# Performance work log

Hardware: AMD Instinct MI355X
Metric: run time of the kernel (lower is better)

Reference implementation:

```python
import jax, jax.numpy as jnp
import numpy as np
import math

DIM, HEAD_DIM = 1024, 64
N_HEADS = DIM // HEAD_DIM
B, S = 8, 1025
EPS = 1e-5


def _make_theta():
    # freqs: geometric between pi and 10*pi
    log_min, log_max = math.log(math.pi), math.log(10 * math.pi)
    n = N_HEADS * HEAD_DIM // 4
    freqs = np.exp(np.linspace(log_min, log_max, n + 1, dtype=np.float64)[:-1]).astype(np.float32)
    freqs = freqs.reshape(HEAD_DIM // 4, N_HEADS).T  # (H, D/4)
    # axial positions on a 32x32 grid, with one zero row prepended -> 1025 rows
    h_pos = np.linspace(-1, 1, 33, dtype=np.float32)
    h_pos = (h_pos[:-1] + h_pos[1:]) / 2
    hh, ww = np.meshgrid(h_pos, h_pos, indexing='ij')
    pos = np.stack([hh, ww], axis=-1).reshape(32 * 32, 2)
    pos = np.concatenate([np.zeros((1, 2), np.float32), pos], axis=0)  # (1025, 2)
    theta_h = pos[:, None, 0:1] * freqs  # (1025, H, D/4)
    theta_w = pos[:, None, 1:2] * freqs
    return jnp.asarray(np.concatenate([theta_h, theta_w], axis=-1))  # (1025, H, D/2)


def _rope(x, theta):
    # x: (B,H,S,D); theta: (B,H,S,d) with d = D//2
    d = theta.shape[-1]
    x1, x2, rest = x[..., :d], x[..., d:2 * d], x[..., 2 * d:]
    cos, sin = jnp.cos(theta), jnp.sin(theta)
    y1 = x1 * cos - x2 * sin
    y2 = x2 * cos + x1 * sin
    return jnp.concatenate([y1, y2, rest], axis=-1)


def setup_inputs() -> dict:
    key = jax.random.key(0)
    ks = jax.random.split(key, 8)
    x = jax.random.normal(ks[0], (B, S, DIM), jnp.float32)
    pos = jax.random.randint(ks[1], (B, S), 0, 1025)
    s = 1.0 / math.sqrt(DIM)
    return {
        'x': x,
        'pos': pos,
        'theta': _make_theta(),
        'ln_w': jnp.ones((DIM,), jnp.float32),
        'ln_b': jnp.zeros((DIM,), jnp.float32),
        'qkv_w': jax.random.normal(ks[2], (3 * DIM, DIM), jnp.float32) * s,
        'qkv_b': jnp.zeros((3 * DIM,), jnp.float32),
        'out_w': jax.random.normal(ks[3], (DIM, DIM), jnp.float32) * (s * 0.02),
        'out_b': jnp.zeros((DIM,), jnp.float32),
    }


def reference(x, pos, theta, ln_w, ln_b, qkv_w, qkv_b, out_w, out_b):
    b, s, dim = x.shape
    # LayerNorm
    mu = jnp.mean(x, axis=-1, keepdims=True)
    var = jnp.mean(jnp.square(x - mu), axis=-1, keepdims=True)
    h = (x - mu) * jax.lax.rsqrt(var + EPS) * ln_w + ln_b
    # QKV projection -> (B, S, 3, H, D)
    qkv = (h @ qkv_w.T + qkv_b).reshape(b, s, 3, N_HEADS, HEAD_DIM)
    q = qkv[:, :, 0].transpose(0, 2, 1, 3)  # (B,H,S,D)
    k = qkv[:, :, 1].transpose(0, 2, 1, 3)
    v = qkv[:, :, 2].transpose(0, 2, 1, 3)
    # Rotary: theta[pos] -> (B,S,H,d) -> (B,H,S,d)
    th = theta[pos].transpose(0, 2, 1, 3)
    q = _rope(q, th)
    k = _rope(k, th)
    # causal SDPA
    scale = 1.0 / math.sqrt(HEAD_DIM)
    scores = jnp.einsum('bhqd,bhkd->bhqk', q, k) * scale
    causal = jnp.tril(jnp.ones((s, s), bool))
    scores = jnp.where(causal, scores, jnp.finfo(scores.dtype).min)
    attn = jax.nn.softmax(scores, axis=-1)
    o = jnp.einsum('bhqk,bhkd->bhqd', attn, v)
    o = o.transpose(0, 2, 1, 3).reshape(b, s, dim)
    return o @ out_w.T + out_b
```

## Files before the change

### kernel.cpp

```cpp
#include <hip/hip_runtime.h>
#include <math.h>

#define B_SZ 8
#define S_LEN 1025
#define DIM 1024
#define NH 16
#define HD 64
#define QKV_DIM 3072
#define M_ROWS (B_SZ * S_LEN)

typedef __attribute__((ext_vector_type(8))) short bf16x8;
typedef __attribute__((ext_vector_type(4))) float f32x4;

__device__ __forceinline__ unsigned short f2bf(float x) {
  unsigned u = __float_as_uint(x);
  unsigned r = u + 0x7FFFu + ((u >> 16) & 1u);
  return (unsigned short)(r >> 16);
}
__device__ __forceinline__ float bf2f(unsigned short h) {
  return __uint_as_float(((unsigned)h) << 16);
}

__device__ __forceinline__ int lds_addr(int row, int byte_in_row) {
  return row * 128 + (byte_in_row & 15) + ((((byte_in_row >> 4) ^ row) & 7) << 4);
}

__device__ __forceinline__ void cvt_write8(char* hi, char* lo, const float* f) {
  union { unsigned short us[8]; uint4 q; } H, L;
  #pragma unroll
  for (int i = 0; i < 8; ++i) {
    unsigned short h = f2bf(f[i]);
    H.us[i] = h;
    L.us[i] = f2bf(f[i] - bf2f(h));
  }
  *(uint4*)hi = H.q;
  *(uint4*)lo = L.q;
}

__global__ __launch_bounds__(256) void ln_kernel(const float* __restrict__ x,
                                                 const float* __restrict__ w,
                                                 const float* __restrict__ b,
                                                 float* __restrict__ h) {
  const int row = blockIdx.x;
  const int t = threadIdx.x;
  const float* xr = x + (size_t)row * DIM;
  float4 v = *(const float4*)(xr + t * 4);
  float s  = v.x + v.y + v.z + v.w;
  float s2 = v.x * v.x + v.y * v.y + v.z * v.z + v.w * v.w;
  #pragma unroll
  for (int off = 32; off > 0; off >>= 1) {
    s  += __shfl_down(s, off);
    s2 += __shfl_down(s2, off);
  }
  __shared__ float red[10];
  const int wid = t >> 6;
  if ((t & 63) == 0) { red[wid] = s; red[4 + wid] = s2; }
  __syncthreads();
  if (t == 0) {
    float ts = 0.f, ts2 = 0.f;
    #pragma unroll
    for (int i = 0; i < 4; ++i) { ts += red[i]; ts2 += red[4 + i]; }
    float mu  = ts * (1.0f / DIM);
    float var = ts2 * (1.0f / DIM) - mu * mu;
    red[8] = mu;
    red[9] = rsqrtf(var + 1e-5f);
  }
  __syncthreads();
  const float mu = red[8], rs = red[9];
  float4 wv = *(const float4*)(w + t * 4);
  float4 bv = *(const float4*)(b + t * 4);
  float4 o;
  o.x = (v.x - mu) * rs * wv.x + bv.x;
  o.y = (v.y - mu) * rs * wv.y + bv.y;
  o.z = (v.z - mu) * rs * wv.z + bv.z;
  o.w = (v.w - mu) * rs * wv.w + bv.w;
  *(float4*)(h + (size_t)row * DIM + t * 4) = o;
}

__global__ __launch_bounds__(256) void gemm_bf16x3(const float* __restrict__ A,
                                                   const float* __restrict__ B,
                                                   const float* __restrict__ bias,
                                                   float* __restrict__ C,
                                                   int M, int N, int K) {
  __shared__ char lds[65536];
  char* Ahi = lds;
  char* Alo = lds + 16384;
  char* Bhi = lds + 32768;
  char* Blo = lds + 49152;

  const int t = threadIdx.x;
  const int l = t & 63;
  const int wid = t >> 6;
  const int wrow = (wid & 1) * 64;
  const int wcol = (wid >> 1) * 64;
  const int m0 = blockIdx.x * 128;
  const int n0 = blockIdx.y * 128;

  const f32x4 zero = {0.f, 0.f, 0.f, 0.f};
  f32x4 acc[4][4];
  #pragma unroll
  for (int i = 0; i < 4; ++i)
    #pragma unroll
    for (int j = 0; j < 4; ++j) acc[i][j] = zero;

  const int kc = (t & 7) * 8;
  const int lrow = (l & 15);
  const int lch = (l >> 4);

  for (int k0 = 0; k0 < K; k0 += 64) {
    __syncthreads();
    float va[4][8], vb[4][8];
    #pragma unroll
    for (int p = 0; p < 4; ++p) {
      const int row = p * 32 + (t >> 3);
      const int m = m0 + row;
      if (m < M) {
        const float* pa = A + (size_t)m * K + k0 + kc;
        *(float4*)&va[p][0] = *(const float4*)pa;
        *(float4*)&va[p][4] = *(const float4*)(pa + 4);
      } else {
        #pragma unroll
        for (int i = 0; i < 8; ++i) va[p][i] = 0.f;
      }
      const float* pb = B + (size_t)(n0 + row) * K + k0 + kc;
      *(float4*)&vb[p][0] = *(const float4*)pb;
      *(float4*)&vb[p][4] = *(const float4*)(pb + 4);
    }
    #pragma unroll
    for (int p = 0; p < 4; ++p) {
      const int row = p * 32 + (t >> 3);
      const int a = lds_addr(row, kc * 2);
      cvt_write8(Ahi + a, Alo + a, va[p]);
      cvt_write8(Bhi + a, Blo + a, vb[p]);
    }
    __syncthreads();
    #pragma unroll
    for (int ks = 0; ks < 2; ++ks) {
      const int bycol = ks * 64 + lch * 16;
      bf16x8 ah[4], al[4], bh[4], bl[4];
      #pragma unroll
      for (int rt = 0; rt < 4; ++rt) {
        const int ar = lds_addr(wrow + rt * 16 + lrow, bycol);
        ah[rt] = *(const bf16x8*)(Ahi + ar);
        al[rt] = *(const bf16x8*)(Alo + ar);
        const int br = lds_addr(wcol + rt * 16 + lrow, bycol);
        bh[rt] = *(const bf16x8*)(Bhi + br);
        bl[rt] = *(const bf16x8*)(Blo + br);
      }
      #pragma unroll
      for (int rt = 0; rt < 4; ++rt)
        #pragma unroll
        for (int ct = 0; ct < 4; ++ct) {
          acc[rt][ct] = __builtin_amdgcn_mfma_f32_16x16x32_bf16(ah[rt], bh[ct], acc[rt][ct], 0, 0, 0);
          acc[rt][ct] = __builtin_amdgcn_mfma_f32_16x16x32_bf16(ah[rt], bl[ct], acc[rt][ct], 0, 0, 0);
          acc[rt][ct] = __builtin_amdgcn_mfma_f32_16x16x32_bf16(al[rt], bh[ct], acc[rt][ct], 0, 0, 0);
        }
    }
  }

  #pragma unroll
  for (int rt = 0; rt < 4; ++rt)
    #pragma unroll
    for (int ct = 0; ct < 4; ++ct) {
      const int n = n0 + wcol + ct * 16 + lrow;
      const float bv = bias[n];
      #pragma unroll
      for (int j = 0; j < 4; ++j) {
        const int m = m0 + wrow + rt * 16 + lch * 4 + j;
        if (m < M) C[(size_t)m * N + n] = acc[rt][ct][j] + bv;
      }
    }
}

__global__ __launch_bounds__(256) void rope_kernel(float* __restrict__ qkv,
                                                   const int* __restrict__ pos,
                                                   const float* __restrict__ theta) {
  const int id = blockIdx.x * 256 + threadIdx.x;
  if (id >= B_SZ * S_LEN * NH * 32) return;
  const int d  = id & 31;
  const int hh = (id >> 5) & 15;
  const int bs = id >> 9;
  const int p = pos[bs];
  const float th = theta[((size_t)p * NH + hh) * 32 + d];
  float sn, c;
  sincosf(th, &sn, &c);
  const size_t base = (size_t)bs * QKV_DIM + hh * HD + d;
  #pragma unroll
  for (int tt = 0; tt < 2; ++tt) {
    const size_t i1 = base + tt * DIM;
    float x1 = qkv[i1];
    float x2 = qkv[i1 + 32];
    qkv[i1]      = x1 * c - x2 * sn;
    qkv[i1 + 32] = x2 * c + x1 * sn;
  }
}

__global__ __launch_bounds__(256) void attn_mfma(const float* __restrict__ qkv,
                                                 float* __restrict__ o_out) {
  const int qt = blockIdx.x;
  const int hh = blockIdx.y;
  const int b  = blockIdx.z;
  const int t  = threadIdx.x;
  const int l  = t & 63;
  const int w  = t >> 6;
  const int q0 = qt * 64;
  const int lrow = l & 15;
  const int lch  = l >> 4;

  __shared__ char lds[49152];
  char* Khi  = lds;
  char* Klo  = lds + 8192;
  char* Vthi = lds + 16384;
  char* Vtlo = lds + 24576;
  char* Phi  = lds + 32768;
  char* Plo  = lds + 40960;

  const size_t bs_base = (size_t)b * S_LEN * QKV_DIM;

  bf16x8 qh[2], ql[2];
  {
    const int qrow = q0 + w * 16 + lrow;
    #pragma unroll
    for (int ks = 0; ks < 2; ++ks) {
      float f[8];
      if (qrow < S_LEN) {
        const float* p = qkv + bs_base + (size_t)qrow * QKV_DIM + hh * HD + ks * 32 + lch * 8;
        *(float4*)&f[0] = *(const float4*)p;
        *(float4*)&f[4] = *(const float4*)(p + 4);
      } else {
        #pragma unroll
        for (int i = 0; i < 8; ++i) f[i] = 0.f;
      }
      union { unsigned short us[8]; bf16x8 v; } H, L;
      #pragma unroll
      for (int i = 0; i < 8; ++i) {
        const float x = f[i] * 0.125f;
        unsigned short hi = f2bf(x);
        H.us[i] = hi;
        L.us[i] = f2bf(x - bf2f(hi));
      }
      qh[ks] = H.v;
      ql[ks] = L.v;
    }
  }

  const f32x4 zero = {0.f, 0.f, 0.f, 0.f};
  f32x4 acc[4];
  float m[4], lsum[4];
  #pragma unroll
  for (int ct = 0; ct < 4; ++ct) acc[ct] = zero;
  #pragma unroll
  for (int j = 0; j < 4; ++j) { m[j] = -1e30f; lsum[j] = 0.f; }

  const int kt_max = (q0 + 63 < S_LEN ? q0 + 63 : S_LEN - 1) >> 6;
  const int sr = t >> 2;
  const int sg = t & 3;

  for (int kt = 0; kt <= kt_max; ++kt) {
    const int k0 = kt * 64;
    __syncthreads();
    {
      float kf[16], vf[16];
      const int s = k0 + sr;
      if (s < S_LEN) {
        const float* base = qkv + bs_base + (size_t)s * QKV_DIM + hh * HD + sg * 16;
        #pragma unroll
        for (int q = 0; q < 4; ++q) {
          *(float4*)&kf[q * 4] = *(const float4*)(base + DIM + q * 4);
          *(float4*)&vf[q * 4] = *(const float4*)(base + 2 * DIM + q * 4);
        }
      } else {
        #pragma unroll
        for (int i = 0; i < 16; ++i) { kf[i] = 0.f; vf[i] = 0.f; }
      }
      const int a0 = lds_addr(sr, sg * 32);
      const int a1 = lds_addr(sr, sg * 32 + 16);
      cvt_write8(Khi + a0, Klo + a0, kf);
      cvt_write8(Khi + a1, Klo + a1, kf + 8);
      #pragma unroll
      for (int i = 0; i < 16; ++i) {
        const int ad = lds_addr(sg * 16 + i, sr * 2);
        unsigned short hi = f2bf(vf[i]);
        *(unsigned short*)(Vthi + ad) = hi;
        *(unsigned short*)(Vtlo + ad) = f2bf(vf[i] - bf2f(hi));
      }
    }
    __syncthreads();

    f32x4 sc[4];
    #pragma unroll
    for (int ct = 0; ct < 4; ++ct) {
      f32x4 s = zero;
      #pragma unroll
      for (int ks = 0; ks < 2; ++ks) {
        const int off = lds_addr(ct * 16 + lrow, ks * 64 + lch * 16);
        bf16x8 kh = *(const bf16x8*)(Khi + off);
        bf16x8 kl = *(const bf16x8*)(Klo + off);
        s = __builtin_amdgcn_mfma_f32_16x16x32_bf16(qh[ks], kh, s, 0, 0, 0);
        s = __builtin_amdgcn_mfma_f32_16x16x32_bf16(qh[ks], kl, s, 0, 0, 0);
        s = __builtin_amdgcn_mfma_f32_16x16x32_bf16(ql[ks], kh, s, 0, 0, 0);
      }
      sc[ct] = s;
    }

    #pragma unroll
    for (int ct = 0; ct < 4; ++ct) {
      const int kj = k0 + lrow + ct * 16;
      #pragma unroll
      for (int j = 0; j < 4; ++j) {
        const int qi = q0 + w * 16 + lch * 4 + j;
        if (kj > qi) sc[ct][j] = -1e30f;
      }
    }

    float tmax[4];
    #pragma unroll
    for (int j = 0; j < 4; ++j)
      tmax[j] = fmaxf(fmaxf(sc[0][j], sc[1][j]), fmaxf(sc[2][j], sc[3][j]));
    #pragma unroll
    for (int off = 1; off < 16; off <<= 1)
      #pragma unroll
      for (int j = 0; j < 4; ++j)
        tmax[j] = fmaxf(tmax[j], __shfl_xor(tmax[j], off, 16));

    float mnew[4], tsum[4];
    #pragma unroll
    for (int j = 0; j < 4; ++j) {
      mnew[j] = fmaxf(m[j], tmax[j]);
      float su = 0.f;
      #pragma unroll
      for (int ct = 0; ct < 4; ++ct) {
        sc[ct][j] = __expf(sc[ct][j] - mnew[j]);
        su += sc[ct][j];
      }
      tsum[j] = su;
    }
    #pragma unroll
    for (int off = 1; off < 16; off <<= 1)
      #pragma unroll
      for (int j = 0; j < 4; ++j) tsum[j] += __shfl_xor(tsum[j], off, 16);
    #pragma unroll
    for (int j = 0; j < 4; ++j) {
      const float co = __expf(m[j] - mnew[j]);
      lsum[j] = lsum[j] * co + tsum[j];
      #pragma unroll
      for (int ct = 0; ct < 4; ++ct) acc[ct][j] *= co;
      m[j] = mnew[j];
    }

    #pragma unroll
    for (int ct = 0; ct < 4; ++ct)
      #pragma unroll
      for (int j = 0; j < 4; ++j) {
        const float pv = sc[ct][j];
        const int ad = lds_addr(w * 16 + lch * 4 + j, (lrow + ct * 16) * 2);
        unsigned short hi = f2bf(pv);
        *(unsigned short*)(Phi + ad) = hi;
        *(unsigned short*)(Plo + ad) = f2bf(pv - bf2f(hi));
      }
    __syncthreads();

    #pragma unroll
    for (int ks = 0; ks < 2; ++ks) {
      const int poff = lds_addr(w * 16 + lrow, ks * 64 + lch * 16);
      bf16x8 ph = *(const bf16x8*)(Phi + poff);
      bf16x8 pl = *(const bf16x8*)(Plo + poff);
      #pragma unroll
      for (int ct = 0; ct < 4; ++ct) {
        const int voff = lds_addr(ct * 16 + lrow, ks * 64 + lch * 16);
        bf16x8 vh = *(const bf16x8*)(Vthi + voff);
        bf16x8 vl = *(const bf16x8*)(Vtlo + voff);
        acc[ct] = __builtin_amdgcn_mfma_f32_16x16x32_bf16(ph, vh, acc[ct], 0, 0, 0);
        acc[ct] = __builtin_amdgcn_mfma_f32_16x16x32_bf16(ph, vl, acc[ct], 0, 0, 0);
        acc[ct] = __builtin_amdgcn_mfma_f32_16x16x32_bf16(pl, vh, acc[ct], 0, 0, 0);
      }
    }
  }

  #pragma unroll
  for (int j = 0; j < 4; ++j) {
    const int s = q0 + w * 16 + lch * 4 + j;
    if (s >= S_LEN) continue;
    const float inv = 1.f / lsum[j];
    #pragma unroll
    for (int ct = 0; ct < 4; ++ct)
      o_out[((size_t)b * S_LEN + s) * DIM + hh * HD + lrow + ct * 16] = acc[ct][j] * inv;
  }
}

extern "C" void kernel_launch(void* const* d_in, const int* in_sizes, int n_in,
                              void* d_out, int out_size, void* d_ws, size_t ws_size,
                              hipStream_t stream) {
  const float* x     = (const float*)d_in[0];
  const int*   pos   = (const int*)d_in[1];
  const float* theta = (const float*)d_in[2];
  const float* ln_w  = (const float*)d_in[3];
  const float* ln_b  = (const float*)d_in[4];
  const float* qkv_w = (const float*)d_in[5];
  const float* qkv_b = (const float*)d_in[6];
  const float* out_w = (const float*)d_in[7];
  const float* out_b = (const float*)d_in[8];
  float* out = (float*)d_out;

  float* h   = (float*)d_ws;
  float* qkv = h + (size_t)M_ROWS * DIM;
  float* o   = h;

  ln_kernel<<<M_ROWS, 256, 0, stream>>>(x, ln_w, ln_b, h);
  gemm_bf16x3<<<dim3(65, 24), 256, 0, stream>>>(h, qkv_w, qkv_b, qkv,
                                                M_ROWS, QKV_DIM, DIM);
  rope_kernel<<<(B_SZ * S_LEN * NH * 32 + 255) / 256, 256, 0, stream>>>(qkv, pos, theta);
  attn_mfma<<<dim3(17, NH, B_SZ), 256, 0, stream>>>(qkv, o);
  gemm_bf16x3<<<dim3(65, 8), 256, 0, stream>>>(o, out_w, out_b, out,
                                               M_ROWS, DIM, DIM);
}
```

Baseline: 632.2 us.

## Store intermediates as pre-split bf16 hi/lo planes across all kernels

LayerNorm, the QKV GEMM epilogue, rope and attention output now write activations as separate bf16 hi and lo planes, not fp32. Consumers load these planes straight into LDS and skip the per-tile fp32-to-bf16x2 split, which cuts conversion ALU work in the GEMM and attention K/V loading loops. The Q scale moves from the Q load to the scores. Total bytes per element stay the same, but the QKV epilogue does uncoalesced 2-byte stores and rope does extra split work.

```diff
diff --git a/kernel.cpp b/kernel.cpp
--- a/kernel.cpp
+++ b/kernel.cpp
@@ -1,4 +1,5 @@
 #include <hip/hip_runtime.h>
+#include <hip/hip_bf16.h>
 #include <math.h>
 
 #define B_SZ 8
@@ -11,13 +12,15 @@
 
 typedef __attribute__((ext_vector_type(8))) short bf16x8;
 typedef __attribute__((ext_vector_type(4))) float f32x4;
-
-__device__ __forceinline__ unsigned short f2bf(float x) {
-  unsigned u = __float_as_uint(x);
-  unsigned r = u + 0x7FFFu + ((u >> 16) & 1u);
-  return (unsigned short)(r >> 16);
-}
-__device__ __forceinline__ float bf2f(unsigned short h) {
+typedef unsigned short u16;
+
+__device__ __forceinline__ void bsplit(float x, u16& hi, u16& lo) {
+  __hip_bfloat16 bh = __float2bfloat16(x);
+  __builtin_memcpy(&hi, &bh, 2);
+  __hip_bfloat16 bl = __float2bfloat16(x - __bfloat162float(bh));
+  __builtin_memcpy(&lo, &bl, 2);
+}
+__device__ __forceinline__ float bf2f(u16 h) {
   return __uint_as_float(((unsigned)h) << 16);
 }
 
@@ -25,14 +28,10 @@
   return row * 128 + (byte_in_row & 15) + ((((byte_in_row >> 4) ^ row) & 7) << 4);
 }
 
-__device__ __forceinline__ void cvt_write8(char* hi, char* lo, const float* f) {
-  union { unsigned short us[8]; uint4 q; } H, L;
-  #pragma unroll
-  for (int i = 0; i < 8; ++i) {
-    unsigned short h = f2bf(f[i]);
-    H.us[i] = h;
-    L.us[i] = f2bf(f[i] - bf2f(h));
-  }
+__device__ __forceinline__ void split_write8(char* hi, char* lo, const float* f) {
+  union { u16 us[8]; uint4 q; } H, L;
+  #pragma unroll
+  for (int i = 0; i < 8; ++i) bsplit(f[i], H.us[i], L.us[i]);
   *(uint4*)hi = H.q;
   *(uint4*)lo = L.q;
 }
@@ -40,7 +39,8 @@
 __global__ __launch_bounds__(256) void ln_kernel(const float* __restrict__ x,
                                                  const float* __restrict__ w,
                                                  const float* __restrict__ b,
-                                                 float* __restrict__ h) {
+                                                 u16* __restrict__ h_hi,
+                                                 u16* __restrict__ h_lo) {
   const int row = blockIdx.x;
   const int t = threadIdx.x;
   const float* xr = x + (size_t)row * DIM;
@@ -69,19 +69,27 @@
   const float mu = red[8], rs = red[9];
   float4 wv = *(const float4*)(w + t * 4);
   float4 bv = *(const float4*)(b + t * 4);
-  float4 o;
-  o.x = (v.x - mu) * rs * wv.x + bv.x;
-  o.y = (v.y - mu) * rs * wv.y + bv.y;
-  o.z = (v.z - mu) * rs * wv.z + bv.z;
-  o.w = (v.w - mu) * rs * wv.w + bv.w;
-  *(float4*)(h + (size_t)row * DIM + t * 4) = o;
-}
-
-__global__ __launch_bounds__(256) void gemm_bf16x3(const float* __restrict__ A,
-                                                   const float* __restrict__ B,
-                                                   const float* __restrict__ bias,
-                                                   float* __restrict__ C,
-                                                   int M, int N, int K) {
+  float o[4];
+  o[0] = (v.x - mu) * rs * wv.x + bv.x;
+  o[1] = (v.y - mu) * rs * wv.y + bv.y;
+  o[2] = (v.z - mu) * rs * wv.z + bv.z;
+  o[3] = (v.w - mu) * rs * wv.w + bv.w;
+  union { u16 us[4]; uint2 q; } H, L;
+  #pragma unroll
+  for (int i = 0; i < 4; ++i) bsplit(o[i], H.us[i], L.us[i]);
+  *(uint2*)(h_hi + (size_t)row * DIM + t * 4) = H.q;
+  *(uint2*)(h_lo + (size_t)row * DIM + t * 4) = L.q;
+}
+
+template <bool PLANES_OUT>
+__global__ __launch_bounds__(256) void gemm_ps(const u16* __restrict__ Ahi_g,
+                                               const u16* __restrict__ Alo_g,
+                                               const float* __restrict__ B,
+                                               const float* __restrict__ bias,
+                                               float* __restrict__ Cf,
+                                               u16* __restrict__ Chi,
+                                               u16* __restrict__ Clo,
+                                               int M, int N, int K) {
   __shared__ char lds[65536];
   char* Ahi = lds;
   char* Alo = lds + 16384;
@@ -109,29 +117,29 @@
 
   for (int k0 = 0; k0 < K; k0 += 64) {
     __syncthreads();
-    float va[4][8], vb[4][8];
     #pragma unroll
     for (int p = 0; p < 4; ++p) {
       const int row = p * 32 + (t >> 3);
       const int m = m0 + row;
+      uint4 vh = make_uint4(0, 0, 0, 0), vl = make_uint4(0, 0, 0, 0);
       if (m < M) {
-        const float* pa = A + (size_t)m * K + k0 + kc;
-        *(float4*)&va[p][0] = *(const float4*)pa;
-        *(float4*)&va[p][4] = *(const float4*)(pa + 4);
-      } else {
-        #pragma unroll
-        for (int i = 0; i < 8; ++i) va[p][i] = 0.f;
-      }
-      const float* pb = B + (size_t)(n0 + row) * K + k0 + kc;
-      *(float4*)&vb[p][0] = *(const float4*)pb;
-      *(float4*)&vb[p][4] = *(const float4*)(pb + 4);
+        const size_t off = (size_t)m * K + k0 + kc;
+        vh = *(const uint4*)(Ahi_g + off);
+        vl = *(const uint4*)(Alo_g + off);
+      }
+      const int a = lds_addr(row, kc * 2);
+      *(uint4*)(Ahi + a) = vh;
+      *(uint4*)(Alo + a) = vl;
     }
     #pragma unroll
     for (int p = 0; p < 4; ++p) {
       const int row = p * 32 + (t >> 3);
+      float vb[8];
+      const float* pb = B + (size_t)(n0 + row) * K + k0 + kc;
+      *(float4*)&vb[0] = *(const float4*)pb;
+      *(float4*)&vb[4] = *(const float4*)(pb + 4);
       const int a = lds_addr(row, kc * 2);
-      cvt_write8(Ahi + a, Alo + a, va[p]);
-      cvt_write8(Bhi + a, Blo + a, vb[p]);
+      split_write8(Bhi + a, Blo + a, vb);
     }
     __syncthreads();
     #pragma unroll
@@ -167,12 +175,23 @@
       #pragma unroll
       for (int j = 0; j < 4; ++j) {
         const int m = m0 + wrow + rt * 16 + lch * 4 + j;
-        if (m < M) C[(size_t)m * N + n] = acc[rt][ct][j] + bv;
-      }
-    }
-}
-
-__global__ __launch_bounds__(256) void rope_kernel(float* __restrict__ qkv,
+        if (m >= M) continue;
+        const float val = acc[rt][ct][j] + bv;
+        const size_t idx = (size_t)m * N + n;
+        if (PLANES_OUT) {
+          u16 hu, lu;
+          bsplit(val, hu, lu);
+          Chi[idx] = hu;
+          Clo[idx] = lu;
+        } else {
+          Cf[idx] = val;
+        }
+      }
+    }
+}
+
+__global__ __launch_bounds__(256) void rope_planes(u16* __restrict__ qkv_hi,
+                                                   u16* __restrict__ qkv_lo,
                                                    const int* __restrict__ pos,
                                                    const float* __restrict__ theta) {
   const int id = blockIdx.x * 256 + threadIdx.x;
@@ -188,15 +207,19 @@
   #pragma unroll
   for (int tt = 0; tt < 2; ++tt) {
     const size_t i1 = base + tt * DIM;
-    float x1 = qkv[i1];
-    float x2 = qkv[i1 + 32];
-    qkv[i1]      = x1 * c - x2 * sn;
-    qkv[i1 + 32] = x2 * c + x1 * sn;
-  }
-}
-
-__global__ __launch_bounds__(256) void attn_mfma(const float* __restrict__ qkv,
-                                                 float* __restrict__ o_out) {
+    const float x1 = bf2f(qkv_hi[i1]) + bf2f(qkv_lo[i1]);
+    const float x2 = bf2f(qkv_hi[i1 + 32]) + bf2f(qkv_lo[i1 + 32]);
+    const float y1 = x1 * c - x2 * sn;
+    const float y2 = x2 * c + x1 * sn;
+    bsplit(y1, qkv_hi[i1], qkv_lo[i1]);
+    bsplit(y2, qkv_hi[i1 + 32], qkv_lo[i1 + 32]);
+  }
+}
+
+__global__ __launch_bounds__(256) void attn_mfma(const u16* __restrict__ qkv_hi,
+                                                 const u16* __restrict__ qkv_lo,
+                                                 u16* __restrict__ o_hi,
+                                                 u16* __restrict__ o_lo) {
   const int qt = blockIdx.x;
   const int hh = blockIdx.y;
   const int b  = blockIdx.z;
@@ -222,25 +245,14 @@
     const int qrow = q0 + w * 16 + lrow;
     #pragma unroll
     for (int ks = 0; ks < 2; ++ks) {
-      float f[8];
       if (qrow < S_LEN) {
-        const float* p = qkv + bs_base + (size_t)qrow * QKV_DIM + hh * HD + ks * 32 + lch * 8;
-        *(float4*)&f[0] = *(const float4*)p;
-        *(float4*)&f[4] = *(const float4*)(p + 4);
+        const size_t off = bs_base + (size_t)qrow * QKV_DIM + hh * HD + ks * 32 + lch * 8;
+        qh[ks] = *(const bf16x8*)(qkv_hi + off);
+        ql[ks] = *(const bf16x8*)(qkv_lo + off);
       } else {
-        #pragma unroll
-        for (int i = 0; i < 8; ++i) f[i] = 0.f;
-      }
-      union { unsigned short us[8]; bf16x8 v; } H, L;
-      #pragma unroll
-      for (int i = 0; i < 8; ++i) {
-        const float x = f[i] * 0.125f;
-        unsigned short hi = f2bf(x);
-        H.us[i] = hi;
-        L.us[i] = f2bf(x - bf2f(hi));
-      }
-      qh[ks] = H.v;
-      ql[ks] = L.v;
+        qh[ks] = (bf16x8)(short)0;
+        ql[ks] = (bf16x8)(short)0;
+      }
     }
   }
 
@@ -260,29 +272,32 @@
     const int k0 = kt * 64;
     __syncthreads();
     {
-      float kf[16], vf[16];
+      uint4 kh0 = make_uint4(0,0,0,0), kh1 = kh0, kl0 = kh0, kl1 = kh0;
+      union { uint4 q[2]; u16 us[16]; } VH, VL;
+      VH.q[0] = VH.q[1] = VL.q[0] = VL.q[1] = make_uint4(0,0,0,0);
       const int s = k0 + sr;
       if (s < S_LEN) {
-        const float* base = qkv + bs_base + (size_t)s * QKV_DIM + hh * HD + sg * 16;
-        #pragma unroll
-        for (int q = 0; q < 4; ++q) {
-          *(float4*)&kf[q * 4] = *(const float4*)(base + DIM + q * 4);
-          *(float4*)&vf[q * 4] = *(const float4*)(base + 2 * DIM + q * 4);
-        }
-      } else {
-        #pragma unroll
-        for (int i = 0; i < 16; ++i) { kf[i] = 0.f; vf[i] = 0.f; }
+        const size_t off = bs_base + (size_t)s * QKV_DIM + hh * HD + sg * 16;
+        kh0 = *(const uint4*)(qkv_hi + off + DIM);
+        kh1 = *(const uint4*)(qkv_hi + off + DIM + 8);
+        kl0 = *(const uint4*)(qkv_lo + off + DIM);
+        kl1 = *(const uint4*)(qkv_lo + off + DIM + 8);
+        VH.q[0] = *(const uint4*)(qkv_hi + off + 2 * DIM);
+        VH.q[1] = *(const uint4*)(qkv_hi + off + 2 * DIM + 8);
+        VL.q[0] = *(const uint4*)(qkv_lo + off + 2 * DIM);
+        VL.q[1] = *(const uint4*)(qkv_lo + off + 2 * DIM + 8);
       }
       const int a0 = lds_addr(sr, sg * 32);
       const int a1 = lds_addr(sr, sg * 32 + 16);
-      cvt_write8(Khi + a0, Klo + a0, kf);
-      cvt_write8(Khi + a1, Klo + a1, kf + 8);
+      *(uint4*)(Khi + a0) = kh0;
+      *(uint4*)(Khi + a1) = kh1;
+      *(uint4*)(Klo + a0) = kl0;
+      *(uint4*)(Klo + a1) = kl1;
       #pragma unroll
       for (int i = 0; i < 16; ++i) {
         const int ad = lds_addr(sg * 16 + i, sr * 2);
-        unsigned short hi = f2bf(vf[i]);
-        *(unsigned short*)(Vthi + ad) = hi;
-        *(unsigned short*)(Vtlo + ad) = f2bf(vf[i] - bf2f(hi));
+        *(u16*)(Vthi + ad) = VH.us[i];
+        *(u16*)(Vtlo + ad) = VL.us[i];
       }
     }
     __syncthreads();
@@ -300,6 +315,8 @@
         s = __builtin_amdgcn_mfma_f32_16x16x32_bf16(qh[ks], kl, s, 0, 0, 0);
         s = __builtin_amdgcn_mfma_f32_16x16x32_bf16(ql[ks], kh, s, 0, 0, 0);
       }
+      #pragma unroll
+      for (int j = 0; j < 4; ++j) s[j] *= 0.125f;
       sc[ct] = s;
     }
 
@@ -352,11 +369,11 @@
     for (int ct = 0; ct < 4; ++ct)
       #pragma unroll
       for (int j = 0; j < 4; ++j) {
-        const float pv = sc[ct][j];
         const int ad = lds_addr(w * 16 + lch * 4 + j, (lrow + ct * 16) * 2);
-        unsigned short hi = f2bf(pv);
-        *(unsigned short*)(Phi + ad) = hi;
-        *(unsigned short*)(Plo + ad) = f2bf(pv - bf2f(hi));
+        u16 hu, lu;
+        bsplit(sc[ct][j], hu, lu);
+        *(u16*)(Phi + ad) = hu;
+        *(u16*)(Plo + ad) = lu;
       }
     __syncthreads();
 
@@ -383,8 +400,13 @@
     if (s >= S_LEN) continue;
     const float inv = 1.f / lsum[j];
     #pragma unroll
-    for (int ct = 0; ct < 4; ++ct)
-      o_out[((size_t)b * S_LEN + s) * DIM + hh * HD + lrow + ct * 16] = acc[ct][j] * inv;
+    for (int ct = 0; ct < 4; ++ct) {
+      const size_t idx = ((size_t)b * S_LEN + s) * DIM + hh * HD + lrow + ct * 16;
+      u16 hu, lu;
+      bsplit(acc[ct][j] * inv, hu, lu);
+      o_hi[idx] = hu;
+      o_lo[idx] = lu;
+    }
   }
 }
 
@@ -402,15 +424,20 @@
   const float* out_b = (const float*)d_in[8];
   float* out = (float*)d_out;
 
-  float* h   = (float*)d_ws;
-  float* qkv = h + (size_t)M_ROWS * DIM;
-  float* o   = h;
-
-  ln_kernel<<<M_ROWS, 256, 0, stream>>>(x, ln_w, ln_b, h);
-  gemm_bf16x3<<<dim3(65, 24), 256, 0, stream>>>(h, qkv_w, qkv_b, qkv,
-                                                M_ROWS, QKV_DIM, DIM);
-  rope_kernel<<<(B_SZ * S_LEN * NH * 32 + 255) / 256, 256, 0, stream>>>(qkv, pos, theta);
-  attn_mfma<<<dim3(17, NH, B_SZ), 256, 0, stream>>>(qkv, o);
-  gemm_bf16x3<<<dim3(65, 8), 256, 0, stream>>>(o, out_w, out_b, out,
-                                               M_ROWS, DIM, DIM);
-}
+  u16* h_hi   = (u16*)d_ws;
+  u16* h_lo   = h_hi + (size_t)M_ROWS * DIM;
+  u16* qkv_hi = h_lo + (size_t)M_ROWS * DIM;
+  u16* qkv_lo = qkv_hi + (size_t)M_ROWS * QKV_DIM;
+  u16* o_hi   = h_hi;
+  u16* o_lo   = h_lo;
+
+  ln_kernel<<<M_ROWS, 256, 0, stream>>>(x, ln_w, ln_b, h_hi, h_lo);
+  gemm_ps<true><<<dim3(65, 24), 256, 0, stream>>>(h_hi, h_lo, qkv_w, qkv_b,
+                                                  nullptr, qkv_hi, qkv_lo,
+                                                  M_ROWS, QKV_DIM, DIM);
+  rope_planes<<<(B_SZ * S_LEN * NH * 32 + 255) / 256, 256, 0, stream>>>(qkv_hi, qkv_lo, pos, theta);
+  attn_mfma<<<dim3(17, NH, B_SZ), 256, 0, stream>>>(qkv_hi, qkv_lo, o_hi, o_lo);
+  gemm_ps<false><<<dim3(65, 8), 256, 0, stream>>>(o_hi, o_lo, out_w, out_b,
+                                                  out, nullptr, nullptr,
+                                                  M_ROWS, DIM, DIM);
+}
```

Result: no change. 632.0 us (-0.0%).
